# Performance work log

Measured on AMD Instinct MI355X. Metric: run time of the kernel, lower is better.

## Reference

```python
import jax, jax.numpy as jnp
import numpy as np

KSIZE = 3
RES_SCALE = 0.2
WITH_RESIDUAL = True


def setup_inputs() -> dict:
    key = jax.random.key(0)
    x = jax.random.normal(key, (8, 3, 1024, 1024), dtype=jnp.float32)
    return {"x": x}


def reference(x) -> jnp.ndarray:
    B, C, H, W = x.shape
    k = KSIZE
    p = k // 2
    # zero padding matches F.unfold(padding=k//2)
    xp = jnp.pad(x, ((0, 0), (0, 0), (p, p), (p, p)))
    # [B, C, k*k, H, W] stack of shifted views (k*k = 9, small static loop)
    patches = jnp.stack(
        [xp[:, :, di:di + H, dj:dj + W] for di in range(k) for dj in range(k)],
        axis=2,
    )
    # median of odd-sized window = middle element of sorted values
    med = jnp.sort(patches, axis=2)[:, :, (k * k) // 2]
    if WITH_RESIDUAL:
        return x + RES_SCALE * (med - x)
    return med
```

## Files before the change

kernel.cpp:

```cpp
#include <hip/hip_runtime.h>


typedef float v4f __attribute__((ext_vector_type(4)));

#define S2(a,b) { float _t=fminf(a,b); (b)=fmaxf(a,b); (a)=_t; }
__device__ __forceinline__ float med3f(float a, float b, float c) {
    return fmaxf(fminf(a, b), fminf(fmaxf(a, b), c));
}

constexpr int W = 1024, H = 1024;

__global__ __launch_bounds__(256, 6) void median_blur_kernel(
    const float* __restrict__ xin, float* __restrict__ out)
{
    const unsigned orig  = blockIdx.x;
    const unsigned chunk = gridDim.x >> 3;
    const unsigned wg    = (orig & 7u) * chunk + (orig >> 3);

    const int tx   = threadIdx.x;
    const int wv   = tx >> 6;
    const int lane = tx & 63;

    const unsigned g = wg * 4u + (unsigned)wv;
    const int    y     = (int)(g & 1023u);
    const size_t plane = (size_t)(g >> 10) * (size_t)(H * W);
    const float* base  = xin + plane;

    const int yt = y > 0     ? y - 1 : 0;
    const int yb = y < H - 1 ? y + 1 : H - 1;
    const float* rpt = base + ((size_t)yt << 10);
    const float* rpm = base + ((size_t)y  << 10);
    const float* rpb = base + ((size_t)yb << 10);

    const int xo = lane << 2;

    v4f ct[4], cm[4], cb[4];
#pragma unroll
    for (int j = 0; j < 4; ++j) {
        ct[j] = *reinterpret_cast<const v4f*>(rpt + (j << 8) + xo);
        cm[j] = *reinterpret_cast<const v4f*>(rpm + (j << 8) + xo);
        cb[j] = *reinterpret_cast<const v4f*>(rpb + (j << 8) + xo);
    }

    if (y == 0) {
#pragma unroll
        for (int j = 0; j < 4; ++j) ct[j] = (v4f){0.0f, 0.0f, 0.0f, 0.0f};
    }
    if (y == H - 1) {
#pragma unroll
        for (int j = 0; j < 4; ++j) cb[j] = (v4f){0.0f, 0.0f, 0.0f, 0.0f};
    }

    float* o_row = out + plane + ((size_t)y << 10);

#pragma unroll
    for (int j = 0; j < 4; ++j) {
        float tl_u = __shfl_up(ct[j].w, 1), ml_u = __shfl_up(cm[j].w, 1), bl_u = __shfl_up(cb[j].w, 1);
        float tl_b = (j > 0) ? __shfl(ct[j - 1].w, 63) : 0.0f;
        float ml_b = (j > 0) ? __shfl(cm[j - 1].w, 63) : 0.0f;
        float bl_b = (j > 0) ? __shfl(cb[j - 1].w, 63) : 0.0f;
        const float tl = (lane == 0) ? tl_b : tl_u;
        const float ml = (lane == 0) ? ml_b : ml_u;
        const float bl = (lane == 0) ? bl_b : bl_u;
        float tr_d = __shfl_down(ct[j].x, 1), mr_d = __shfl_down(cm[j].x, 1), br_d = __shfl_down(cb[j].x, 1);
        float tr_b = (j < 3) ? __shfl(ct[j + 1].x, 0) : 0.0f;
        float mr_b = (j < 3) ? __shfl(cm[j + 1].x, 0) : 0.0f;
        float br_b = (j < 3) ? __shfl(cb[j + 1].x, 0) : 0.0f;
        const float tr = (lane == 63) ? tr_b : tr_d;
        const float mr = (lane == 63) ? mr_b : mr_d;
        const float br = (lane == 63) ? br_b : br_d;

        const float t[6] = { tl, ct[j].x, ct[j].y, ct[j].z, ct[j].w, tr };
        const float m[6] = { ml, cm[j].x, cm[j].y, cm[j].z, cm[j].w, mr };
        const float b[6] = { bl, cb[j].x, cb[j].y, cb[j].z, cb[j].w, br };

        float lo[6], mi[6], hi[6];
#pragma unroll
        for (int q = 0; q < 6; ++q) {
            float a = t[q], c0 = m[q], d = b[q];
            S2(a, c0); S2(c0, d); S2(a, c0);
            lo[q] = a; mi[q] = c0; hi[q] = d;
        }
        v4f o;
#pragma unroll
        for (int q = 0; q < 4; ++q) {
            const float mxlo = fmaxf(lo[q], fmaxf(lo[q + 1], lo[q + 2]));
            const float mnhi = fminf(hi[q], fminf(hi[q + 1], hi[q + 2]));
            const float mdmi = med3f(mi[q], mi[q + 1], mi[q + 2]);
            const float med  = med3f(mxlo, mdmi, mnhi);
            const float xc   = m[q + 1];
            o[q] = xc + 0.2f * (med - xc);
        }
        *reinterpret_cast<v4f*>(o_row + (j << 8) + xo) = o;
    }
}

extern "C" void kernel_launch(void* const* d_in, const int* in_sizes, int n_in,
                              void* d_out, int out_size, void* d_ws, size_t ws_size,
                              hipStream_t stream) {
    const float* x = (const float*)d_in[0];
    float* out = (float*)d_out;
    const int planes = in_sizes[0] / (H * W);
    dim3 block(256);
    dim3 grid(planes * (H / 4));
    median_blur_kernel<<<grid, block, 0, stream>>>(x, out);
}
```

Before: 174.3 us.

## Process four rows per wave with register row reuse and chunk prefetch

Each wave now computes four consecutive output rows from six loaded input rows, so the vertical halo is no longer re-read for every row. Column chunks are double-buffered so the next chunk's loads are issued before the current chunk is computed. The left halo is carried across chunks through a shuffle. The grid shrinks fourfold, and register pressure grows, which may lower occupancy.

```diff
diff --git a/kernel.cpp b/kernel.cpp
--- a/kernel.cpp
+++ b/kernel.cpp
@@ -9,89 +9,97 @@
 }
 
 constexpr int W = 1024, H = 1024;
+constexpr int RPW = 4;
+constexpr int NRW = RPW + 2;
 
 __global__ __launch_bounds__(256, 6) void median_blur_kernel(
     const float* __restrict__ xin, float* __restrict__ out)
 {
-    const unsigned orig  = blockIdx.x;
-    const unsigned chunk = gridDim.x >> 3;
-    const unsigned wg    = (orig & 7u) * chunk + (orig >> 3);
+    const unsigned orig   = blockIdx.x;
+    const unsigned chunkB = gridDim.x >> 3;
+    const unsigned wg     = (orig & 7u) * chunkB + (orig >> 3);
 
     const int tx   = threadIdx.x;
     const int wv   = tx >> 6;
     const int lane = tx & 63;
 
     const unsigned g = wg * 4u + (unsigned)wv;
-    const int    y     = (int)(g & 1023u);
-    const size_t plane = (size_t)(g >> 10) * (size_t)(H * W);
+    const int    y0    = (int)((g & 255u) << 2);
+    const size_t plane = (size_t)(g >> 8) * (size_t)(H * W);
     const float* base  = xin + plane;
+    float*       obase = out + plane;
 
-    const int yt = y > 0     ? y - 1 : 0;
-    const int yb = y < H - 1 ? y + 1 : H - 1;
-    const float* rpt = base + ((size_t)yt << 10);
-    const float* rpm = base + ((size_t)y  << 10);
-    const float* rpb = base + ((size_t)yb << 10);
+    const bool top = (y0 == 0);
+    const bool bot = (y0 == H - RPW);
+
+    const float* rp[NRW];
+#pragma unroll
+    for (int s = 0; s < NRW; ++s) {
+        int y = y0 - 1 + s;
+        y = y < 0 ? 0 : (y > H - 1 ? H - 1 : y);
+        rp[s] = base + ((size_t)y << 10);
+    }
 
     const int xo = lane << 2;
 
-    v4f ct[4], cm[4], cb[4];
+    v4f   c[2][NRW];
+    float carry[NRW];
 #pragma unroll
-    for (int j = 0; j < 4; ++j) {
-        ct[j] = *reinterpret_cast<const v4f*>(rpt + (j << 8) + xo);
-        cm[j] = *reinterpret_cast<const v4f*>(rpm + (j << 8) + xo);
-        cb[j] = *reinterpret_cast<const v4f*>(rpb + (j << 8) + xo);
-    }
+    for (int s = 0; s < NRW; ++s) carry[s] = 0.0f;
 
-    if (y == 0) {
 #pragma unroll
-        for (int j = 0; j < 4; ++j) ct[j] = (v4f){0.0f, 0.0f, 0.0f, 0.0f};
-    }
-    if (y == H - 1) {
-#pragma unroll
-        for (int j = 0; j < 4; ++j) cb[j] = (v4f){0.0f, 0.0f, 0.0f, 0.0f};
-    }
-
-    float* o_row = out + plane + ((size_t)y << 10);
+    for (int s = 0; s < NRW; ++s)
+        c[0][s] = *reinterpret_cast<const v4f*>(rp[s] + xo);
+    if (top) c[0][0]       = (v4f){0.0f, 0.0f, 0.0f, 0.0f};
+    if (bot) c[0][NRW - 1] = (v4f){0.0f, 0.0f, 0.0f, 0.0f};
 
 #pragma unroll
     for (int j = 0; j < 4; ++j) {
-        float tl_u = __shfl_up(ct[j].w, 1), ml_u = __shfl_up(cm[j].w, 1), bl_u = __shfl_up(cb[j].w, 1);
-        float tl_b = (j > 0) ? __shfl(ct[j - 1].w, 63) : 0.0f;
-        float ml_b = (j > 0) ? __shfl(cm[j - 1].w, 63) : 0.0f;
-        float bl_b = (j > 0) ? __shfl(cb[j - 1].w, 63) : 0.0f;
-        const float tl = (lane == 0) ? tl_b : tl_u;
-        const float ml = (lane == 0) ? ml_b : ml_u;
-        const float bl = (lane == 0) ? bl_b : bl_u;
-        float tr_d = __shfl_down(ct[j].x, 1), mr_d = __shfl_down(cm[j].x, 1), br_d = __shfl_down(cb[j].x, 1);
-        float tr_b = (j < 3) ? __shfl(ct[j + 1].x, 0) : 0.0f;
-        float mr_b = (j < 3) ? __shfl(cm[j + 1].x, 0) : 0.0f;
-        float br_b = (j < 3) ? __shfl(cb[j + 1].x, 0) : 0.0f;
-        const float tr = (lane == 63) ? tr_b : tr_d;
-        const float mr = (lane == 63) ? mr_b : mr_d;
-        const float br = (lane == 63) ? br_b : br_d;
+        const int cur = j & 1, nxt = cur ^ 1;
+        if (j < 3) {
+#pragma unroll
+            for (int s = 0; s < NRW; ++s)
+                c[nxt][s] = *reinterpret_cast<const v4f*>(rp[s] + ((j + 1) << 8) + xo);
+            if (top) c[nxt][0]       = (v4f){0.0f, 0.0f, 0.0f, 0.0f};
+            if (bot) c[nxt][NRW - 1] = (v4f){0.0f, 0.0f, 0.0f, 0.0f};
+        }
 
-        const float t[6] = { tl, ct[j].x, ct[j].y, ct[j].z, ct[j].w, tr };
-        const float m[6] = { ml, cm[j].x, cm[j].y, cm[j].z, cm[j].w, mr };
-        const float b[6] = { bl, cb[j].x, cb[j].y, cb[j].z, cb[j].w, br };
+        float hl[NRW], hr[NRW];
+#pragma unroll
+        for (int s = 0; s < NRW; ++s) {
+            const float u  = __shfl_up(c[cur][s].w, 1);
+            hl[s] = (lane == 0) ? carry[s] : u;
+            const float d  = __shfl_down(c[cur][s].x, 1);
+            const float nb = (j < 3) ? __shfl(c[nxt][s].x, 0) : 0.0f;
+            hr[s] = (lane == 63) ? nb : d;
+            carry[s] = __shfl(c[cur][s].w, 63);
+        }
 
-        float lo[6], mi[6], hi[6];
 #pragma unroll
-        for (int q = 0; q < 6; ++q) {
-            float a = t[q], c0 = m[q], d = b[q];
-            S2(a, c0); S2(c0, d); S2(a, c0);
-            lo[q] = a; mi[q] = c0; hi[q] = d;
+        for (int r = 0; r < RPW; ++r) {
+            const float t[6] = { hl[r],     c[cur][r].x,     c[cur][r].y,     c[cur][r].z,     c[cur][r].w,     hr[r]     };
+            const float m[6] = { hl[r + 1], c[cur][r + 1].x, c[cur][r + 1].y, c[cur][r + 1].z, c[cur][r + 1].w, hr[r + 1] };
+            const float b[6] = { hl[r + 2], c[cur][r + 2].x, c[cur][r + 2].y, c[cur][r + 2].z, c[cur][r + 2].w, hr[r + 2] };
+
+            float lo[6], mi[6], hi[6];
+#pragma unroll
+            for (int q = 0; q < 6; ++q) {
+                float a = t[q], c0 = m[q], d = b[q];
+                S2(a, c0); S2(c0, d); S2(a, c0);
+                lo[q] = a; mi[q] = c0; hi[q] = d;
+            }
+            v4f o;
+#pragma unroll
+            for (int q = 0; q < 4; ++q) {
+                const float mxlo = fmaxf(lo[q], fmaxf(lo[q + 1], lo[q + 2]));
+                const float mnhi = fminf(hi[q], fminf(hi[q + 1], hi[q + 2]));
+                const float mdmi = med3f(mi[q], mi[q + 1], mi[q + 2]);
+                const float med  = med3f(mxlo, mdmi, mnhi);
+                const float xc   = m[q + 1];
+                o[q] = xc + 0.2f * (med - xc);
+            }
+            *reinterpret_cast<v4f*>(obase + ((size_t)(y0 + r) << 10) + (j << 8) + xo) = o;
         }
-        v4f o;
-#pragma unroll
-        for (int q = 0; q < 4; ++q) {
-            const float mxlo = fmaxf(lo[q], fmaxf(lo[q + 1], lo[q + 2]));
-            const float mnhi = fminf(hi[q], fminf(hi[q + 1], hi[q + 2]));
-            const float mdmi = med3f(mi[q], mi[q + 1], mi[q + 2]);
-            const float med  = med3f(mxlo, mdmi, mnhi);
-            const float xc   = m[q + 1];
-            o[q] = xc + 0.2f * (med - xc);
-        }
-        *reinterpret_cast<v4f*>(o_row + (j << 8) + xo) = o;
     }
 }
 
@@ -102,6 +110,6 @@
     float* out = (float*)d_out;
     const int planes = in_sizes[0] / (H * W);
     dim3 block(256);
-    dim3 grid(planes * (H / 4));
+    dim3 grid(planes * (H / 16));
     median_blur_kernel<<<grid, block, 0, stream>>>(x, out);
 }
```

Measured after the change: 191.6 us. 9.9% more time.
